# Kernel optimization log

Measured on AMD Instinct MI355X. Metric: run time of the kernel, lower is better.

The kernel has to match this reference:

```python
import jax, jax.numpy as jnp
import numpy as np

NFEAT = 256
N_HEAD = 8
CTXS = (31, 61)
HPS = N_HEAD // len(CTXS)  # heads per scale = 4


def _scale_out(query, value, W1, W2, W3, ctx):
    # query, value: [B, T, F]; W1: [F, F]; W2: [F, HPS*ctx]; W3: [F, F]
    B, T, F = query.shape
    q = jnp.maximum(query @ W1, 0.0)                      # relu(w1(query))
    attn = jax.nn.softmax((q @ W2).reshape(B, T, HPS, ctx), axis=-1)  # [B,T,HPS,ctx]
    half = (ctx - 1) // 2
    v = jnp.pad(value @ W3, ((0, 0), (half, half), (0, 0)))  # [B, T+ctx-1, F]
    idx = jnp.arange(T)[:, None] + jnp.arange(ctx)[None, :]  # [T, ctx] window indices
    vw = v[:, idx]                                          # [B, T, ctx, F]
    vw = vw.reshape(B, T, ctx, HPS, F // HPS)               # per-head dim = F/HPS
    out = jnp.einsum('bthc,btchd->bthd', attn, vw)          # [B,T,HPS,F/HPS]
    return out.reshape(B, T, F)


def setup_inputs() -> dict:
    key = jax.random.key(0)
    ks = jax.random.split(key, 12)
    B, T, F = 2, 4096, NFEAT
    s = 0.02
    return {
        'query': jax.random.normal(ks[0], (B, T, F), jnp.float32),
        'key':   jax.random.normal(ks[1], (B, T, F), jnp.float32),
        'value': jax.random.normal(ks[2], (B, T, F), jnp.float32),
        'w1_0': jax.random.normal(ks[3], (F, F), jnp.float32) * s,
        'w1_1': jax.random.normal(ks[4], (F, F), jnp.float32) * s,
        'w2_0': jax.random.normal(ks[5], (F, HPS * CTXS[0]), jnp.float32) * s,
        'w2_1': jax.random.normal(ks[6], (F, HPS * CTXS[1]), jnp.float32) * s,
        'w3_0': jax.random.normal(ks[7], (F, F), jnp.float32) * s,
        'w3_1': jax.random.normal(ks[8], (F, F), jnp.float32) * s,
        'scale_w': jnp.ones((2,), jnp.float32) / 2.0,
        'w_out': jax.random.normal(ks[9], (F, F), jnp.float32) * s,
    }


def reference(query, key, value, w1_0, w1_1, w2_0, w2_1, w3_0, w3_1, scale_w, w_out):
    sw = jax.nn.softmax(scale_w)
    out = sw[0] * _scale_out(query, value, w1_0, w2_0, w3_0, CTXS[0])
    out = out + sw[1] * _scale_out(query, value, w1_1, w2_1, w3_1, CTXS[1])
    return out @ w_out
```

## Files before the change

kernel.cpp:

```cpp
#include <hip/hip_runtime.h>
#include <hip/hip_bf16.h>
#include <type_traits>

static constexpr int BATCH = 2;
static constexpr int T     = 4096;
static constexpr int F     = 256;
static constexpr int M     = BATCH * T;
static constexpr int K     = 256;
static constexpr int HPS   = 4;
static constexpr int CTX0  = 31, CTX1 = 61;
static constexpr int N2_0  = HPS * CTX0;
static constexpr int N2_1  = HPS * CTX1;

typedef short bf16x8 __attribute__((ext_vector_type(8)));
typedef float f32x4  __attribute__((ext_vector_type(4)));

__device__ __forceinline__ ushort f2bf(float f) {
    union { float f; uint u; } v; v.f = f;
    uint u = v.u;
    return (ushort)((u + 0x7fffu + ((u >> 16) & 1u)) >> 16);
}
__device__ __forceinline__ float bf2f(ushort u) {
    union { uint u; float f; } v; v.u = ((uint)u) << 16;
    return v.f;
}

struct WcvtArgs {
    const float* w1_0; const float* w1_1;
    const float* w2_0; const float* w2_1;
    const float* w3_0; const float* w3_1;
    const float* wo;
    ushort* wt;
};
static constexpr int WT_ROWS = 512 + N2_0 + N2_1 + 512 + 256;

__global__ __launch_bounds__(256) void wcvt_kernel(WcvtArgs a) {
    int gid = blockIdx.x * 256 + threadIdx.x;
    if (gid >= WT_ROWS * (K / 8)) return;
    int row = gid >> 5;
    int kk  = (gid & 31) * 8;

    const float* src; int stride, col;
    if (row < 512) {
        int n = row;
        if (n < 256) { src = a.w1_0; col = n; } else { src = a.w1_1; col = n - 256; }
        stride = 256;
    } else if (row < 512 + N2_0) {
        src = a.w2_0; col = row - 512; stride = N2_0;
    } else if (row < 512 + N2_0 + N2_1) {
        src = a.w2_1; col = row - (512 + N2_0); stride = N2_1;
    } else if (row < 512 + N2_0 + N2_1 + 512) {
        int n = row - (512 + N2_0 + N2_1);
        if (n < 256) { src = a.w3_0; col = n; } else { src = a.w3_1; col = n - 256; }
        stride = 256;
    } else {
        src = a.wo; col = row - (512 + N2_0 + N2_1 + 512); stride = 256;
    }

    ushort o[8];
#pragma unroll
    for (int j = 0; j < 8; j++) o[j] = f2bf(src[(size_t)(kk + j) * stride + col]);
    *reinterpret_cast<bf16x8*>(a.wt + (size_t)row * K + kk) =
        *reinterpret_cast<bf16x8*>(o);
}

template <typename InT, typename OutT, bool RELU>
__global__ __launch_bounds__(256) void gemm_kernel(
    const InT*    __restrict__ A,
    int lda,
    const ushort* __restrict__ Bt,
    OutT*         __restrict__ C,
    int N)
{
    constexpr int BM = 64, BN = 64, BK = 32;
    constexpr int LDA = BK + 8;
    constexpr int LDB = K + 8;
    __shared__ ushort Alds[BM][LDA];
    __shared__ ushort Btl [BN][LDB];

    const int tid = threadIdx.x;
    const int m0 = blockIdx.x * BM;
    const int n0 = blockIdx.y * BN;

    for (int idx = tid; idx < BN * (K / 8); idx += 256) {
        int n  = idx >> 5;
        int kk = (idx & 31) * 8;
        bf16x8 v = {};
        if (n0 + n < N)
            v = *reinterpret_cast<const bf16x8*>(Bt + (size_t)(n0 + n) * K + kk);
        *reinterpret_cast<bf16x8*>(&Btl[n][kk]) = v;
    }

    const int wave = tid >> 6, lane = tid & 63;
    const int wr = wave >> 1, wc = wave & 1;
    const int l15 = lane & 15, l4 = lane >> 4;

    f32x4 acc[2][2] = {};
    __syncthreads();

    for (int k0 = 0; k0 < K; k0 += BK) {
        {
            int row = tid >> 2;
            int kk  = (tid & 3) * 8;
            const InT* ap = A + (size_t)(m0 + row) * lda + k0 + kk;
            if constexpr (std::is_same<InT, float>::value) {
                float4 v0 = *reinterpret_cast<const float4*>(ap);
                float4 v1 = *reinterpret_cast<const float4*>(ap + 4);
                ushort o[8] = { f2bf(v0.x), f2bf(v0.y), f2bf(v0.z), f2bf(v0.w),
                                f2bf(v1.x), f2bf(v1.y), f2bf(v1.z), f2bf(v1.w) };
                *reinterpret_cast<bf16x8*>(&Alds[row][kk]) = *reinterpret_cast<bf16x8*>(o);
            } else {
                *reinterpret_cast<bf16x8*>(&Alds[row][kk]) =
                    *reinterpret_cast<const bf16x8*>(ap);
            }
        }
        __syncthreads();

        bf16x8 af[2], bfr[2];
#pragma unroll
        for (int i = 0; i < 2; i++)
            af[i] = *reinterpret_cast<const bf16x8*>(&Alds[wr * 32 + i * 16 + l15][l4 * 8]);
#pragma unroll
        for (int j = 0; j < 2; j++)
            bfr[j] = *reinterpret_cast<const bf16x8*>(&Btl[wc * 32 + j * 16 + l15][k0 + l4 * 8]);
#pragma unroll
        for (int i = 0; i < 2; i++)
#pragma unroll
            for (int j = 0; j < 2; j++)
                acc[i][j] = __builtin_amdgcn_mfma_f32_16x16x32_bf16(af[i], bfr[j], acc[i][j], 0, 0, 0);
        __syncthreads();
    }

#pragma unroll
    for (int i = 0; i < 2; i++)
#pragma unroll
        for (int j = 0; j < 2; j++) {
            int col = n0 + wc * 32 + j * 16 + l15;
            if (col < N) {
#pragma unroll
                for (int r = 0; r < 4; r++) {
                    int row = m0 + wr * 32 + i * 16 + l4 * 4 + r;
                    float v = acc[i][j][r];
                    if (RELU) v = fmaxf(v, 0.0f);
                    if constexpr (std::is_same<OutT, ushort>::value)
                        C[(size_t)row * N + col] = f2bf(v);
                    else
                        C[(size_t)row * N + col] = v;
                }
            }
        }
}

__global__ __launch_bounds__(256) void attn_kernel(
    const float*  __restrict__ lg0,
    const float*  __restrict__ lg1,
    const ushort* __restrict__ v01,
    const float*  __restrict__ scale_w,
    ushort*       __restrict__ outc)
{
    const int bt0 = blockIdx.x * 8;
    const int tid = threadIdx.x;

    __shared__ float attw[8][368];

    float s0 = scale_w[0], s1 = scale_w[1];
    float mxs = fmaxf(s0, s1);
    float e0 = __expf(s0 - mxs), e1 = __expf(s1 - mxs);
    float sw0 = e0 / (e0 + e1), sw1 = e1 / (e0 + e1);

    {
        int task = tid >> 2, sub = tid & 3;
        int tok = task >> 3, rest = task & 7;
        int scale = rest >> 2, h = rest & 3;
        int bt = bt0 + tok;
        const float* lp;
        float* dst;
        int ctx;
        float sw;
        if (scale == 0) {
            lp  = lg0 + (size_t)bt * N2_0 + h * CTX0;
            dst = &attw[tok][h * CTX0];
            ctx = CTX0; sw = sw0;
        } else {
            lp  = lg1 + (size_t)bt * N2_1 + h * CTX1;
            dst = &attw[tok][124 + h * CTX1];
            ctx = CTX1; sw = sw1;
        }
        float mx = -1e30f;
        for (int c = sub; c < ctx; c += 4) mx = fmaxf(mx, lp[c]);
        mx = fmaxf(mx, __shfl_xor(mx, 1));
        mx = fmaxf(mx, __shfl_xor(mx, 2));
        float s = 0.f;
        for (int c = sub; c < ctx; c += 4) {
            float e = __expf(lp[c] - mx);
            dst[c] = e;
            s += e;
        }
        s += __shfl_xor(s, 1);
        s += __shfl_xor(s, 2);
        float scl = sw / s;
        for (int c = sub; c < ctx; c += 4) dst[c] *= scl;
    }
    __syncthreads();

    const int tok = tid >> 5;
    const int f0  = (tid & 31) * 8;
    const int h   = f0 >> 6;
    const int bt  = bt0 + tok;
    const int b   = bt >> 12;
    const int t   = bt & (T - 1);

    float acc[8] = {};
    const float* a0 = &attw[tok][h * CTX0];
    const float* a1 = &attw[tok][124 + h * CTX1];

#pragma unroll 4
    for (int c = 0; c < CTX0; c++) {
        int tt = t + c - (CTX0 - 1) / 2;
        if ((unsigned)tt < (unsigned)T) {
            bf16x8 v = *reinterpret_cast<const bf16x8*>(
                v01 + ((size_t)(b * T + tt) * 512 + f0));
            float w = a0[c];
#pragma unroll
            for (int j = 0; j < 8; j++) acc[j] += w * bf2f((ushort)v[j]);
        }
    }
#pragma unroll 4
    for (int c = 0; c < CTX1; c++) {
        int tt = t + c - (CTX1 - 1) / 2;
        if ((unsigned)tt < (unsigned)T) {
            bf16x8 v = *reinterpret_cast<const bf16x8*>(
                v01 + ((size_t)(b * T + tt) * 512 + 256 + f0));
            float w = a1[c];
#pragma unroll
            for (int j = 0; j < 8; j++) acc[j] += w * bf2f((ushort)v[j]);
        }
    }

    ushort o[8];
#pragma unroll
    for (int j = 0; j < 8; j++) o[j] = f2bf(acc[j]);
    *reinterpret_cast<bf16x8*>(outc + (size_t)bt * F + f0) =
        *reinterpret_cast<bf16x8*>(o);
}

extern "C" void kernel_launch(void* const* d_in, const int* in_sizes, int n_in,
                              void* d_out, int out_size, void* d_ws, size_t ws_size,
                              hipStream_t stream)
{
    const float* Q    = (const float*)d_in[0];
    const float* V    = (const float*)d_in[2];
    const float* W1_0 = (const float*)d_in[3];
    const float* W1_1 = (const float*)d_in[4];
    const float* W2_0 = (const float*)d_in[5];
    const float* W2_1 = (const float*)d_in[6];
    const float* W3_0 = (const float*)d_in[7];
    const float* W3_1 = (const float*)d_in[8];
    const float* SW   = (const float*)d_in[9];
    const float* WO   = (const float*)d_in[10];

    char* p = (char*)d_ws;
    auto carve = [&](size_t bytes) { char* r = p; p += (bytes + 255) & ~255ull; return r; };
    ushort* wt   = (ushort*)carve((size_t)WT_ROWS * K * 2);
    ushort* q01  = (ushort*)carve((size_t)M * 512 * 2);
    float*  lg0  = (float*) carve((size_t)M * N2_0 * 4);
    float*  lg1  = (float*) carve((size_t)M * N2_1 * 4);
    ushort* v01  = (ushort*)carve((size_t)M * 512 * 2);
    ushort* ocb  = (ushort*)carve((size_t)M * F * 2);
    (void)ws_size;

    const ushort* w1t  = wt;
    const ushort* w2t0 = wt + (size_t)512 * K;
    const ushort* w2t1 = wt + (size_t)(512 + N2_0) * K;
    const ushort* w3t  = wt + (size_t)(512 + N2_0 + N2_1) * K;
    const ushort* wot  = wt + (size_t)(512 + N2_0 + N2_1 + 512) * K;

    {
        WcvtArgs wa { W1_0, W1_1, W2_0, W2_1, W3_0, W3_1, WO, wt };
        int nthread = WT_ROWS * (K / 8);
        wcvt_kernel<<<(nthread + 255) / 256, 256, 0, stream>>>(wa);
    }

    auto grid = [](int N) { return dim3(M / 64, (N + 63) / 64); };

    gemm_kernel<float, ushort, true><<<grid(512), 256, 0, stream>>>(Q, K, w1t, q01, 512);

    gemm_kernel<ushort, float, false><<<grid(N2_0), 256, 0, stream>>>(q01,       512, w2t0, lg0, N2_0);
    gemm_kernel<ushort, float, false><<<grid(N2_1), 256, 0, stream>>>(q01 + 256, 512, w2t1, lg1, N2_1);

    gemm_kernel<float, ushort, false><<<grid(512), 256, 0, stream>>>(V, K, w3t, v01, 512);

    attn_kernel<<<M / 8, 256, 0, stream>>>(lg0, lg1, v01, SW, ocb);

    gemm_kernel<ushort, float, false><<<grid(F), 256, 0, stream>>>(ocb, K, wot, (float*)d_out, F);
}
```

Before: 173.2 us.

## Pre-convert inputs to bf16, load full-K tiles with swizzled LDS, stage value windows

Adds a kernel that converts query and value to bf16 once, instead of reconverting the fp32 A tiles inside every GEMM column block. The GEMM now loads the whole 64x256 A and B tiles into XOR-swizzled LDS once, dropping the per-k-step barriers, and remaps block indices with an XCD-style swizzle. The attention kernel stages the value window rows for its 8 tokens into LDS, replacing repeated global loads and bounds checks, and unpacks bf16 pairs with shifts and masks. The cost is an extra launch, extra workspace traffic for the bf16 copies, and higher LDS use per block, which may lower occupancy.

```diff
diff --git a/kernel.cpp b/kernel.cpp
--- a/kernel.cpp
+++ b/kernel.cpp
@@ -20,9 +20,22 @@
     uint u = v.u;
     return (ushort)((u + 0x7fffu + ((u >> 16) & 1u)) >> 16);
 }
-__device__ __forceinline__ float bf2f(ushort u) {
-    union { uint u; float f; } v; v.u = ((uint)u) << 16;
-    return v.f;
+__device__ __forceinline__ float asf(uint u) {
+    union { uint u; float f; } v; v.u = u; return v.f;
+}
+
+__global__ __launch_bounds__(256) void cvtqv_kernel(
+    const float* __restrict__ q, const float* __restrict__ v,
+    ushort* __restrict__ qb, ushort* __restrict__ vb)
+{
+    const float* src = blockIdx.y ? v : q;
+    ushort*      dst = blockIdx.y ? vb : qb;
+    size_t i = ((size_t)blockIdx.x * 256 + threadIdx.x) * 8;
+    float4 a = *reinterpret_cast<const float4*>(src + i);
+    float4 b = *reinterpret_cast<const float4*>(src + i + 4);
+    ushort o[8] = { f2bf(a.x), f2bf(a.y), f2bf(a.z), f2bf(a.w),
+                    f2bf(b.x), f2bf(b.y), f2bf(b.z), f2bf(b.w) };
+    *reinterpret_cast<bf16x8*>(dst + i) = *reinterpret_cast<bf16x8*>(o);
 }
 
 struct WcvtArgs {
@@ -64,31 +77,38 @@
         *reinterpret_cast<bf16x8*>(o);
 }
 
-template <typename InT, typename OutT, bool RELU>
+template <typename OutT, bool RELU>
 __global__ __launch_bounds__(256) void gemm_kernel(
-    const InT*    __restrict__ A,
+    const ushort* __restrict__ A,
     int lda,
     const ushort* __restrict__ Bt,
     OutT*         __restrict__ C,
-    int N)
+    int N, int ncb)
 {
-    constexpr int BM = 64, BN = 64, BK = 32;
-    constexpr int LDA = BK + 8;
-    constexpr int LDB = K + 8;
-    __shared__ ushort Alds[BM][LDA];
-    __shared__ ushort Btl [BN][LDB];
+    __shared__ ushort Al[64][256];
+    __shared__ ushort Bl[64][256];
 
     const int tid = threadIdx.x;
-    const int m0 = blockIdx.x * BM;
-    const int n0 = blockIdx.y * BN;
-
-    for (int idx = tid; idx < BN * (K / 8); idx += 256) {
-        int n  = idx >> 5;
-        int kk = (idx & 31) * 8;
+    const int nwg = gridDim.x;
+    const int lin = blockIdx.x;
+    const int qq  = nwg >> 3;
+    const int swz = (lin & 7) * qq + (lin >> 3);
+    const int cb  = swz % ncb;
+    const int rb  = swz / ncb;
+    const int m0  = rb * 64;
+    const int n0  = cb * 64;
+
+    for (int idx = tid; idx < 64 * 32; idx += 256) {
+        int row = idx >> 5, ch = idx & 31;
+        bf16x8 v = *reinterpret_cast<const bf16x8*>(A + (size_t)(m0 + row) * lda + ch * 8);
+        *reinterpret_cast<bf16x8*>(&Al[row][(ch ^ (row & 7)) * 8]) = v;
+    }
+    for (int idx = tid; idx < 64 * 32; idx += 256) {
+        int row = idx >> 5, ch = idx & 31;
         bf16x8 v = {};
-        if (n0 + n < N)
-            v = *reinterpret_cast<const bf16x8*>(Bt + (size_t)(n0 + n) * K + kk);
-        *reinterpret_cast<bf16x8*>(&Btl[n][kk]) = v;
+        if (n0 + row < N)
+            v = *reinterpret_cast<const bf16x8*>(Bt + (size_t)(n0 + row) * K + ch * 8);
+        *reinterpret_cast<bf16x8*>(&Bl[row][(ch ^ (row & 7)) * 8]) = v;
     }
 
     const int wave = tid >> 6, lane = tid & 63;
@@ -98,37 +118,26 @@
     f32x4 acc[2][2] = {};
     __syncthreads();
 
-    for (int k0 = 0; k0 < K; k0 += BK) {
-        {
-            int row = tid >> 2;
-            int kk  = (tid & 3) * 8;
-            const InT* ap = A + (size_t)(m0 + row) * lda + k0 + kk;
-            if constexpr (std::is_same<InT, float>::value) {
-                float4 v0 = *reinterpret_cast<const float4*>(ap);
-                float4 v1 = *reinterpret_cast<const float4*>(ap + 4);
-                ushort o[8] = { f2bf(v0.x), f2bf(v0.y), f2bf(v0.z), f2bf(v0.w),
-                                f2bf(v1.x), f2bf(v1.y), f2bf(v1.z), f2bf(v1.w) };
-                *reinterpret_cast<bf16x8*>(&Alds[row][kk]) = *reinterpret_cast<bf16x8*>(o);
-            } else {
-                *reinterpret_cast<bf16x8*>(&Alds[row][kk]) =
-                    *reinterpret_cast<const bf16x8*>(ap);
-            }
-        }
-        __syncthreads();
-
+#pragma unroll
+    for (int s = 0; s < 8; s++) {
         bf16x8 af[2], bfr[2];
 #pragma unroll
-        for (int i = 0; i < 2; i++)
-            af[i] = *reinterpret_cast<const bf16x8*>(&Alds[wr * 32 + i * 16 + l15][l4 * 8]);
-#pragma unroll
-        for (int j = 0; j < 2; j++)
-            bfr[j] = *reinterpret_cast<const bf16x8*>(&Btl[wc * 32 + j * 16 + l15][k0 + l4 * 8]);
+        for (int i = 0; i < 2; i++) {
+            int row = wr * 32 + i * 16 + l15;
+            int ch  = (s * 4 + l4) ^ (row & 7);
+            af[i] = *reinterpret_cast<const bf16x8*>(&Al[row][ch * 8]);
+        }
+#pragma unroll
+        for (int j = 0; j < 2; j++) {
+            int row = wc * 32 + j * 16 + l15;
+            int ch  = (s * 4 + l4) ^ (row & 7);
+            bfr[j] = *reinterpret_cast<const bf16x8*>(&Bl[row][ch * 8]);
+        }
 #pragma unroll
         for (int i = 0; i < 2; i++)
 #pragma unroll
             for (int j = 0; j < 2; j++)
                 acc[i][j] = __builtin_amdgcn_mfma_f32_16x16x32_bf16(af[i], bfr[j], acc[i][j], 0, 0, 0);
-        __syncthreads();
     }
 
 #pragma unroll
@@ -158,10 +167,34 @@
     const float*  __restrict__ scale_w,
     ushort*       __restrict__ outc)
 {
-    const int bt0 = blockIdx.x * 8;
     const int tid = threadIdx.x;
-
-    __shared__ float attw[8][368];
+    const int nwg = gridDim.x;
+    const int lin = blockIdx.x;
+    const int qq  = nwg >> 3;
+    const int swz = (lin & 7) * qq + (lin >> 3);
+    const int bt0 = swz * 8;
+    const int b   = bt0 >> 12;
+    const int t0  = bt0 & (T - 1);
+
+    __shared__ float  attw[8][368];
+    __shared__ ushort v0l[38][256];
+    __shared__ ushort v1l[68][256];
+
+    for (int idx = tid; idx < 1216 + 2176; idx += 256) {
+        ushort* dst; int tt, srccol;
+        if (idx < 1216) {
+            int row = idx >> 5, ch = idx & 31;
+            dst = &v0l[row][ch * 8]; tt = t0 - 15 + row; srccol = ch * 8;
+        } else {
+            int i2 = idx - 1216;
+            int row = i2 >> 5, ch = i2 & 31;
+            dst = &v1l[row][ch * 8]; tt = t0 - 30 + row; srccol = 256 + ch * 8;
+        }
+        bf16x8 v = {};
+        if ((unsigned)tt < (unsigned)T)
+            v = *reinterpret_cast<const bf16x8*>(v01 + ((size_t)(b * T + tt) * 512 + srccol));
+        *reinterpret_cast<bf16x8*>(dst) = v;
+    }
 
     float s0 = scale_w[0], s1 = scale_w[1];
     float mxs = fmaxf(s0, s1);
@@ -173,18 +206,13 @@
         int tok = task >> 3, rest = task & 7;
         int scale = rest >> 2, h = rest & 3;
         int bt = bt0 + tok;
-        const float* lp;
-        float* dst;
-        int ctx;
-        float sw;
+        const float* lp; float* dst; int ctx; float sw;
         if (scale == 0) {
-            lp  = lg0 + (size_t)bt * N2_0 + h * CTX0;
-            dst = &attw[tok][h * CTX0];
-            ctx = CTX0; sw = sw0;
+            lp = lg0 + (size_t)bt * N2_0 + h * CTX0;
+            dst = &attw[tok][h * CTX0]; ctx = CTX0; sw = sw0;
         } else {
-            lp  = lg1 + (size_t)bt * N2_1 + h * CTX1;
-            dst = &attw[tok][124 + h * CTX1];
-            ctx = CTX1; sw = sw1;
+            lp = lg1 + (size_t)bt * N2_1 + h * CTX1;
+            dst = &attw[tok][124 + h * CTX1]; ctx = CTX1; sw = sw1;
         }
         float mx = -1e30f;
         for (int c = sub; c < ctx; c += 4) mx = fmaxf(mx, lp[c]);
@@ -193,8 +221,7 @@
         float s = 0.f;
         for (int c = sub; c < ctx; c += 4) {
             float e = __expf(lp[c] - mx);
-            dst[c] = e;
-            s += e;
+            dst[c] = e; s += e;
         }
         s += __shfl_xor(s, 1);
         s += __shfl_xor(s, 2);
@@ -206,9 +233,6 @@
     const int tok = tid >> 5;
     const int f0  = (tid & 31) * 8;
     const int h   = f0 >> 6;
-    const int bt  = bt0 + tok;
-    const int b   = bt >> 12;
-    const int t   = bt & (T - 1);
 
     float acc[8] = {};
     const float* a0 = &attw[tok][h * CTX0];
@@ -216,31 +240,27 @@
 
 #pragma unroll 4
     for (int c = 0; c < CTX0; c++) {
-        int tt = t + c - (CTX0 - 1) / 2;
-        if ((unsigned)tt < (unsigned)T) {
-            bf16x8 v = *reinterpret_cast<const bf16x8*>(
-                v01 + ((size_t)(b * T + tt) * 512 + f0));
-            float w = a0[c];
-#pragma unroll
-            for (int j = 0; j < 8; j++) acc[j] += w * bf2f((ushort)v[j]);
-        }
+        float w = a0[c];
+        uint4 u = *reinterpret_cast<const uint4*>(&v0l[tok + c][f0]);
+        acc[0] += w * asf(u.x << 16); acc[1] += w * asf(u.x & 0xffff0000u);
+        acc[2] += w * asf(u.y << 16); acc[3] += w * asf(u.y & 0xffff0000u);
+        acc[4] += w * asf(u.z << 16); acc[5] += w * asf(u.z & 0xffff0000u);
+        acc[6] += w * asf(u.w << 16); acc[7] += w * asf(u.w & 0xffff0000u);
     }
 #pragma unroll 4
     for (int c = 0; c < CTX1; c++) {
-        int tt = t + c - (CTX1 - 1) / 2;
-        if ((unsigned)tt < (unsigned)T) {
-            bf16x8 v = *reinterpret_cast<const bf16x8*>(
-                v01 + ((size_t)(b * T + tt) * 512 + 256 + f0));
-            float w = a1[c];
-#pragma unroll
-            for (int j = 0; j < 8; j++) acc[j] += w * bf2f((ushort)v[j]);
-        }
+        float w = a1[c];
+        uint4 u = *reinterpret_cast<const uint4*>(&v1l[tok + c][f0]);
+        acc[0] += w * asf(u.x << 16); acc[1] += w * asf(u.x & 0xffff0000u);
+        acc[2] += w * asf(u.y << 16); acc[3] += w * asf(u.y & 0xffff0000u);
+        acc[4] += w * asf(u.z << 16); acc[5] += w * asf(u.z & 0xffff0000u);
+        acc[6] += w * asf(u.w << 16); acc[7] += w * asf(u.w & 0xffff0000u);
     }
 
     ushort o[8];
 #pragma unroll
     for (int j = 0; j < 8; j++) o[j] = f2bf(acc[j]);
-    *reinterpret_cast<bf16x8*>(outc + (size_t)bt * F + f0) =
+    *reinterpret_cast<bf16x8*>(outc + (size_t)(bt0 + tok) * F + f0) =
         *reinterpret_cast<bf16x8*>(o);
 }
 
@@ -262,6 +282,8 @@
     char* p = (char*)d_ws;
     auto carve = [&](size_t bytes) { char* r = p; p += (bytes + 255) & ~255ull; return r; };
     ushort* wt   = (ushort*)carve((size_t)WT_ROWS * K * 2);
+    ushort* qbf  = (ushort*)carve((size_t)M * K * 2);
+    ushort* vbf  = (ushort*)carve((size_t)M * K * 2);
     ushort* q01  = (ushort*)carve((size_t)M * 512 * 2);
     float*  lg0  = (float*) carve((size_t)M * N2_0 * 4);
     float*  lg1  = (float*) carve((size_t)M * N2_1 * 4);
@@ -276,21 +298,17 @@
     const ushort* wot  = wt + (size_t)(512 + N2_0 + N2_1 + 512) * K;
 
     {
-        WcvtArgs wa { W1_0, W1_1, W2_0, W2_1, W3_0, W3_1, WO, wt };
+        dim3 g(M * K / 8 / 256, 2);
+        cvtqv_kernel<<<g, 256, 0, stream>>>(Q, V, qbf, vbf);
         int nthread = WT_ROWS * (K / 8);
-        wcvt_kernel<<<(nthread + 255) / 256, 256, 0, stream>>>(wa);
-    }
-
-    auto grid = [](int N) { return dim3(M / 64, (N + 63) / 64); };
-
-    gemm_kernel<float, ushort, true><<<grid(512), 256, 0, stream>>>(Q, K, w1t, q01, 512);
-
-    gemm_kernel<ushort, float, false><<<grid(N2_0), 256, 0, stream>>>(q01,       512, w2t0, lg0, N2_0);
-    gemm_kernel<ushort, float, false><<<grid(N2_1), 256, 0, stream>>>(q01 + 256, 512, w2t1, lg1, N2_1);
-
-    gemm_kernel<float, ushort, false><<<grid(512), 256, 0, stream>>>(V, K, w3t, v01, 512);
-
+        wcvt_kernel<<<(nthread + 255) / 256, 256, 0, stream>>>(
+            WcvtArgs{ W1_0, W1_1, W2_0, W2_1, W3_0, W3_1, WO, wt });
+    }
+
+    gemm_kernel<ushort, true ><<<(M/64) * 8, 256, 0, stream>>>(qbf, K, w1t, q01, 512, 8);
+    gemm_kernel<float,  false><<<(M/64) * 2, 256, 0, stream>>>(q01,       512, w2t0, lg0, N2_0, 2);
+    gemm_kernel<float,  false><<<(M/64) * 4, 256, 0, stream>>>(q01 + 256, 512, w2t1, lg1, N2_1, 4);
+    gemm_kernel<ushort, false><<<(M/64) * 8, 256, 0, stream>>>(vbf, K, w3t, v01, 512, 8);
     attn_kernel<<<M / 8, 256, 0, stream>>>(lg0, lg1, v01, SW, ocb);
-
-    gemm_kernel<ushort, float, false><<<grid(F), 256, 0, stream>>>(ocb, K, wot, (float*)d_out, F);
-}
+    gemm_kernel<float,  false><<<(M/64) * 4, 256, 0, stream>>>(ocb, K, wot, (float*)d_out, F, 4);
+}
```

Result: no change. 170.8 us (-1.3%).
